# Performance work log

Measured on AMD Instinct MI355X. Metric: run time of the kernel, lower is better.

Reference implementation:

```python
import jax, jax.numpy as jnp
import numpy as np
from jax import lax

EPS = 1e-5  # nn.BatchNorm2d default eps


def _binarize_act(x):
    # out = sign(x).detach() - clip(x).detach() + clip(x)  (STE)
    c = jnp.clip(x, -1.0, 1.0)
    return c + lax.stop_gradient(jnp.sign(x) - c)


def _binarize_weight(w):
    # w.data = w.fp.sign().add(0.01).sign()  -> {-1,+1}, zeros map to +1.
    # Autograd in torch sees identity wrt the parameter (data swap), i.e. STE.
    wb = jnp.sign(jnp.sign(w) + 0.01)
    return w + lax.stop_gradient(wb - w)


def setup_inputs() -> dict:
    key = jax.random.key(0)
    k1, k2, k3, k4 = jax.random.split(key, 4)
    N, Cin, Cout, H, W = 16, 32, 32, 256, 256
    return {
        "x": jax.random.normal(k1, (N, Cin, H, W), dtype=jnp.float32),
        "weight": jax.random.normal(k2, (Cout, Cin, 3, 3), dtype=jnp.float32),
        "gamma": jnp.ones((Cout,), dtype=jnp.float32),
        "beta": jnp.zeros((Cout,), dtype=jnp.float32),
        "running_mean": jax.random.normal(k3, (Cout,), dtype=jnp.float32) * 0.1,
        "running_var": jax.random.uniform(k4, (Cout,), dtype=jnp.float32) + 0.5,
    }


def reference(x, weight, gamma, beta, running_mean, running_var):
    xb = _binarize_act(x)
    wb = _binarize_weight(weight)
    # 3x3, stride 1, padding 1 -> SAME spatial size
    out = lax.conv_general_dilated(
        xb, wb,
        window_strides=(1, 1),
        padding=((1, 1), (1, 1)),
        dimension_numbers=("NCHW", "OIHW", "NCHW"),
    )
    # BatchNorm2d (inference form with running stats), then ReLU
    inv = gamma / jnp.sqrt(running_var + EPS)  # [C]
    out = out * inv[None, :, None, None] + (beta - running_mean * inv)[None, :, None, None]
    return jax.nn.relu(out)
```

## Files before the change

kernel.cpp:

```cpp
#include <hip/hip_runtime.h>
#include <stdint.h>

#define NB   16
#define CIN  32
#define COUT 32
#define HH   256
#define WW   256
#define HWSZ (HH * WW)
#define EPSV 1e-5f
#define TWD  264

typedef int v4i  __attribute__((ext_vector_type(4)));
typedef int v16i __attribute__((ext_vector_type(16)));

__global__ __launch_bounds__(288) void pack_w_kernel(
    const float* __restrict__ wt, const float* __restrict__ gamma,
    const float* __restrict__ beta, const float* __restrict__ rmean,
    const float* __restrict__ rvar, uint4* __restrict__ afrag,
    float* __restrict__ c0f) {
    __shared__ uint32_t pws[COUT * 9];
    const int j = threadIdx.x;
    if (j < COUT * 9) {
        const int o = j / 9, t = j % 9;
        uint32_t bits = 0;
#pragma unroll
        for (int c = 0; c < CIN; ++c)
            bits |= (wt[(o * CIN + c) * 9 + t] < 0.f) ? (1u << c) : 0u;
        pws[j] = bits;
    }
    __syncthreads();
    if (j < 64) {
        const int sh = (j & 32) >> 1;
#pragma unroll
        for (int t = 0; t < 9; ++t) {
            const uint32_t chunk = pws[(j & 31) * 9 + t] >> sh;
            uint32_t w[4];
#pragma unroll
            for (int k = 0; k < 4; ++k) {
                const uint32_t y = (((chunk >> (4 * k)) & 0xFu) * 0x204081u) & 0x01010101u;
                w[k] = (y * 0xFEu) | 0x01010101u;
            }
            afrag[t * 64 + j] = make_uint4(w[0], w[1], w[2], w[3]);
        }
    }
    {
        const int cls = j >> 5;
        const int o   = j & 31;
        const int rc = cls / 3, cc = cls % 3;
        int wsum = 0;
#pragma unroll
        for (int dh = 0; dh < 3; ++dh)
#pragma unroll
            for (int dw = 0; dw < 3; ++dw) {
                const bool bad = (rc == 0 && dh == 0) || (rc == 2 && dh == 2) ||
                                 (cc == 0 && dw == 0) || (cc == 2 && dw == 2);
                if (!bad) wsum += 32 - 2 * __popc(pws[o * 9 + dh * 3 + dw]);
            }
        const float inv = gamma[o] * rsqrtf(rvar[o] + EPSV);
        c0f[cls * 32 + o] = beta[o] - rmean[o] * inv + (float)wsum * inv;
        if (cls == 0) c0f[288 + o] = -2.0f * inv;
    }
}

__global__ __launch_bounds__(512) void biconv_mfma(
    const uint32_t* __restrict__ x, const uint4* __restrict__ afrag,
    const float* __restrict__ c0f, float* __restrict__ out) {
    const uint32_t bid = blockIdx.x;
    const uint32_t wg  = ((bid & 7u) << 8) | (bid >> 3);
    const int n   = wg >> 7;
    const int h0  = (wg & 127) << 1;
    const int tid  = threadIdx.x;
    const int lane = tid & 63;
    const int wave = tid >> 6;

    __shared__ uint32_t tiles[4][TWD];
    __shared__ uint4    afsh[9 * 64];
    __shared__ float    csh[320];

    if (tid < 256) {
        const int r  = tid >> 6;
        const int q  = tid & 63;
        const int hr = h0 - 1 + r;
        uint32_t b0 = 0, b1 = 0, b2 = 0, b3 = 0;
        if (hr >= 0 && hr < HH) {
            const uint32_t* xp = x + (size_t)n * (CIN * HWSZ) + (size_t)hr * WW + (q << 2);
#pragma unroll
            for (int c = 0; c < CIN; ++c) {
                const uint4 v = *reinterpret_cast<const uint4*>(xp + (size_t)c * HWSZ);
                b0 |= (v.x >> 31) << c;
                b1 |= (v.y >> 31) << c;
                b2 |= (v.z >> 31) << c;
                b3 |= (v.w >> 31) << c;
            }
        }
        *reinterpret_cast<uint4*>(&tiles[r][(q << 2) + 4]) = make_uint4(b0, b1, b2, b3);
    } else {
        const int t2 = tid - 256;
        afsh[t2]       = afrag[t2];
        afsh[t2 + 256] = afrag[t2 + 256];
        if (t2 < 64)  afsh[t2 + 512] = afrag[t2 + 512];
        csh[t2] = c0f[t2];
        if (t2 < 64)  csh[t2 + 256] = c0f[t2 + 256];
        if (t2 < 8)   tiles[t2 >> 1][(t2 & 1) ? 260 : 3] = 0u;
    }
    __syncthreads();

    const int l31  = lane & 31;
    const int shv  = (lane & 32) >> 1;
    const int og   = (lane >> 5) << 2;
    const int rsel = wave >> 2;
    const int pA   = ((wave & 3) << 6) + l31;
    const int pB   = pA + 32;

    const int h  = h0 + rsel;
    const int rc = (h == 0) ? 0 : ((h == HH - 1) ? 2 : 1);

    v16i acc0 = {0}, acc1 = {0};
#pragma unroll
    for (int dh = 0; dh < 3; ++dh) {
        const uint32_t* trow = &tiles[rsel + dh][0];
#pragma unroll
        for (int dw = 0; dw < 3; ++dw) {
            const v4i a = *reinterpret_cast<const v4i*>(&afsh[(dh * 3 + dw) * 64 + lane]);
            const uint32_t hA = trow[pA + 3 + dw] >> shv;
            const uint32_t hB = trow[pB + 3 + dw] >> shv;
            v4i b;
            b.x = (int)((( hA        & 0xFu) * 0x204081u) & 0x01010101u);
            b.y = (int)((((hA >> 4)  & 0xFu) * 0x204081u) & 0x01010101u);
            b.z = (int)((((hA >> 8)  & 0xFu) * 0x204081u) & 0x01010101u);
            b.w = (int)((((hA >> 12) & 0xFu) * 0x204081u) & 0x01010101u);
            acc0 = __builtin_amdgcn_mfma_i32_32x32x32_i8(a, b, acc0, 0, 0, 0);
            b.x = (int)((( hB        & 0xFu) * 0x204081u) & 0x01010101u);
            b.y = (int)((((hB >> 4)  & 0xFu) * 0x204081u) & 0x01010101u);
            b.z = (int)((((hB >> 8)  & 0xFu) * 0x204081u) & 0x01010101u);
            b.w = (int)((((hB >> 12) & 0xFu) * 0x204081u) & 0x01010101u);
            acc1 = __builtin_amdgcn_mfma_i32_32x32x32_i8(a, b, acc1, 0, 0, 0);
        }
    }

    const int ccA = (pA == 0) ? 0 : ((pA == WW - 1) ? 2 : 1);
    const int ccB = (pB == WW - 1) ? 2 : 1;
    const float* c0A = &csh[(rc * 3 + ccA) * 32];
    const float* c0B = &csh[(rc * 3 + ccB) * 32];
    const float* c1  = &csh[288];
    float* outn = out + (size_t)n * (COUT * HWSZ) + (size_t)h * WW;
#pragma unroll
    for (int e = 0; e < 16; ++e) {
        const int o = (e & 3) + ((e >> 2) << 3) + og;
        const float vA = fmaf((float)acc0[e], c1[o], c0A[o]);
        const float vB = fmaf((float)acc1[e], c1[o], c0B[o]);
        __builtin_nontemporal_store(vA > 0.f ? vA : 0.f, outn + (size_t)o * HWSZ + pA);
        __builtin_nontemporal_store(vB > 0.f ? vB : 0.f, outn + (size_t)o * HWSZ + pB);
    }
}

extern "C" void kernel_launch(void* const* d_in, const int* in_sizes, int n_in,
                              void* d_out, int out_size, void* d_ws, size_t ws_size,
                              hipStream_t stream) {
    const float* x     = (const float*)d_in[0];
    const float* wt    = (const float*)d_in[1];
    const float* gamma = (const float*)d_in[2];
    const float* beta  = (const float*)d_in[3];
    const float* rmean = (const float*)d_in[4];
    const float* rvar  = (const float*)d_in[5];
    float* out = (float*)d_out;

    uint4* afrag = (uint4*)d_ws;
    float* c0f   = (float*)((char*)d_ws + 9216);

    pack_w_kernel<<<dim3(1), dim3(288), 0, stream>>>(wt, gamma, beta, rmean,
                                                     rvar, afrag, c0f);
    biconv_mfma<<<dim3(NB * HH / 2), dim3(512), 0, stream>>>(
        (const uint32_t*)x, afrag, c0f, out);
}
```

Measured before the change: 49.83 us.

## Prepack activation sign bits in a separate kernel before the MFMA conv

Moves the binarization and bit-packing of the input into a separate pre-pass that writes a packed bit buffer (one word per pixel holding 32 channel bits) to the workspace. Each conv block then loads prepacked rows instead of reading every fp32 channel. Before, each input row was read and packed by several blocks (each block loads 4 rows for 2 output rows), so the input was read about twice. The pre-pass uses nontemporal loads and also absorbs the weight packing as an extra block. The cost is one more round trip of a small packed buffer through memory and a dependency between the two launches.

```diff
diff --git a/kernel.cpp b/kernel.cpp
--- a/kernel.cpp
+++ b/kernel.cpp
@@ -9,61 +9,91 @@
 #define HWSZ (HH * WW)
 #define EPSV 1e-5f
 #define TWD  264
+#define NPACKB (NB * HWSZ / 4 / 256)
 
-typedef int v4i  __attribute__((ext_vector_type(4)));
-typedef int v16i __attribute__((ext_vector_type(16)));
+typedef int  v4i  __attribute__((ext_vector_type(4)));
+typedef int  v16i __attribute__((ext_vector_type(16)));
+typedef unsigned int v4u __attribute__((ext_vector_type(4)));
 
-__global__ __launch_bounds__(288) void pack_w_kernel(
-    const float* __restrict__ wt, const float* __restrict__ gamma,
-    const float* __restrict__ beta, const float* __restrict__ rmean,
-    const float* __restrict__ rvar, uint4* __restrict__ afrag,
+__global__ __launch_bounds__(256) void pack_kernel(
+    const uint32_t* __restrict__ x, const float* __restrict__ wt,
+    const float* __restrict__ gamma, const float* __restrict__ beta,
+    const float* __restrict__ rmean, const float* __restrict__ rvar,
+    uint32_t* __restrict__ px, uint4* __restrict__ afrag,
     float* __restrict__ c0f) {
+    const int tid = threadIdx.x;
+    if (blockIdx.x < NPACKB) {
+        const int gt  = blockIdx.x * 256 + tid;
+        const int wi  = gt << 2;
+        const int n   = wi >> 16;
+        const int rem = wi & (HWSZ - 1);
+        const uint32_t* xp = x + (size_t)n * (CIN * HWSZ) + rem;
+        uint32_t b0 = 0, b1 = 0, b2 = 0, b3 = 0;
+#pragma unroll
+        for (int c = 0; c < CIN; ++c) {
+            const v4u v = __builtin_nontemporal_load(
+                reinterpret_cast<const v4u*>(xp + (size_t)c * HWSZ));
+            b0 |= (v.x >> 31) << c;
+            b1 |= (v.y >> 31) << c;
+            b2 |= (v.z >> 31) << c;
+            b3 |= (v.w >> 31) << c;
+        }
+        *reinterpret_cast<uint4*>(px + wi) = make_uint4(b0, b1, b2, b3);
+        return;
+    }
     __shared__ uint32_t pws[COUT * 9];
-    const int j = threadIdx.x;
-    if (j < COUT * 9) {
-        const int o = j / 9, t = j % 9;
-        uint32_t bits = 0;
 #pragma unroll
-        for (int c = 0; c < CIN; ++c)
-            bits |= (wt[(o * CIN + c) * 9 + t] < 0.f) ? (1u << c) : 0u;
-        pws[j] = bits;
+    for (int it = 0; it < 2; ++it) {
+        const int j = tid + it * 256;
+        if (j < COUT * 9) {
+            const int o = j / 9, t = j % 9;
+            uint32_t bits = 0;
+#pragma unroll
+            for (int c = 0; c < CIN; ++c)
+                bits |= (wt[(o * CIN + c) * 9 + t] < 0.f) ? (1u << c) : 0u;
+            pws[j] = bits;
+        }
     }
     __syncthreads();
-    if (j < 64) {
-        const int sh = (j & 32) >> 1;
+    if (tid < 64) {
+        const int sh = (tid & 32) >> 1;
 #pragma unroll
         for (int t = 0; t < 9; ++t) {
-            const uint32_t chunk = pws[(j & 31) * 9 + t] >> sh;
+            const uint32_t chunk = pws[(tid & 31) * 9 + t] >> sh;
             uint32_t w[4];
 #pragma unroll
             for (int k = 0; k < 4; ++k) {
                 const uint32_t y = (((chunk >> (4 * k)) & 0xFu) * 0x204081u) & 0x01010101u;
                 w[k] = (y * 0xFEu) | 0x01010101u;
             }
-            afrag[t * 64 + j] = make_uint4(w[0], w[1], w[2], w[3]);
+            afrag[t * 64 + tid] = make_uint4(w[0], w[1], w[2], w[3]);
         }
     }
-    {
-        const int cls = j >> 5;
-        const int o   = j & 31;
-        const int rc = cls / 3, cc = cls % 3;
-        int wsum = 0;
 #pragma unroll
-        for (int dh = 0; dh < 3; ++dh)
+    for (int it = 0; it < 2; ++it) {
+        const int j = tid + it * 256;
+        if (j < 9 * COUT) {
+            const int cls = j >> 5;
+            const int o   = j & 31;
+            const int rc = cls / 3, cc = cls % 3;
+            int wsum = 0;
 #pragma unroll
-            for (int dw = 0; dw < 3; ++dw) {
-                const bool bad = (rc == 0 && dh == 0) || (rc == 2 && dh == 2) ||
-                                 (cc == 0 && dw == 0) || (cc == 2 && dw == 2);
-                if (!bad) wsum += 32 - 2 * __popc(pws[o * 9 + dh * 3 + dw]);
-            }
-        const float inv = gamma[o] * rsqrtf(rvar[o] + EPSV);
-        c0f[cls * 32 + o] = beta[o] - rmean[o] * inv + (float)wsum * inv;
-        if (cls == 0) c0f[288 + o] = -2.0f * inv;
+            for (int dh = 0; dh < 3; ++dh)
+#pragma unroll
+                for (int dw = 0; dw < 3; ++dw) {
+                    const bool bad = (rc == 0 && dh == 0) || (rc == 2 && dh == 2) ||
+                                     (cc == 0 && dw == 0) || (cc == 2 && dw == 2);
+                    if (!bad) wsum += 32 - 2 * __popc(pws[o * 9 + dh * 3 + dw]);
+                }
+            const float inv = gamma[o] * rsqrtf(rvar[o] + EPSV);
+            c0f[cls * 32 + o] = beta[o] - rmean[o] * inv + (float)wsum * inv;
+            if (cls == 0) c0f[288 + o] = -2.0f * inv;
+        }
     }
 }
 
 __global__ __launch_bounds__(512) void biconv_mfma(
-    const uint32_t* __restrict__ x, const uint4* __restrict__ afrag,
+    const uint32_t* __restrict__ px, const uint4* __restrict__ afrag,
     const float* __restrict__ c0f, float* __restrict__ out) {
     const uint32_t bid = blockIdx.x;
     const uint32_t wg  = ((bid & 7u) << 8) | (bid >> 3);
@@ -81,19 +111,10 @@
         const int r  = tid >> 6;
         const int q  = tid & 63;
         const int hr = h0 - 1 + r;
-        uint32_t b0 = 0, b1 = 0, b2 = 0, b3 = 0;
-        if (hr >= 0 && hr < HH) {
-            const uint32_t* xp = x + (size_t)n * (CIN * HWSZ) + (size_t)hr * WW + (q << 2);
-#pragma unroll
-            for (int c = 0; c < CIN; ++c) {
-                const uint4 v = *reinterpret_cast<const uint4*>(xp + (size_t)c * HWSZ);
-                b0 |= (v.x >> 31) << c;
-                b1 |= (v.y >> 31) << c;
-                b2 |= (v.z >> 31) << c;
-                b3 |= (v.w >> 31) << c;
-            }
-        }
-        *reinterpret_cast<uint4*>(&tiles[r][(q << 2) + 4]) = make_uint4(b0, b1, b2, b3);
+        uint4 v = make_uint4(0u, 0u, 0u, 0u);
+        if (hr >= 0 && hr < HH)
+            v = *reinterpret_cast<const uint4*>(px + (size_t)n * HWSZ + (size_t)hr * WW + (q << 2));
+        *reinterpret_cast<uint4*>(&tiles[r][(q << 2) + 4]) = v;
     } else {
         const int t2 = tid - 256;
         afsh[t2]       = afrag[t2];
@@ -165,11 +186,12 @@
     const float* rvar  = (const float*)d_in[5];
     float* out = (float*)d_out;
 
-    uint4* afrag = (uint4*)d_ws;
-    float* c0f   = (float*)((char*)d_ws + 9216);
+    uint32_t* pxbuf = (uint32_t*)d_ws;
+    uint4*    afrag = (uint4*)(pxbuf + (size_t)NB * HWSZ);
+    float*    c0f   = (float*)((char*)afrag + 9216);
 
-    pack_w_kernel<<<dim3(1), dim3(288), 0, stream>>>(wt, gamma, beta, rmean,
-                                                     rvar, afrag, c0f);
+    pack_kernel<<<dim3(NPACKB + 1), dim3(256), 0, stream>>>(
+        (const uint32_t*)x, wt, gamma, beta, rmean, rvar, pxbuf, afrag, c0f);
     biconv_mfma<<<dim3(NB * HH / 2), dim3(512), 0, stream>>>(
-        (const uint32_t*)x, afrag, c0f, out);
+        pxbuf, afrag, c0f, out);
 }
```

After: 55.43 us. +11.3%, slower.
